# Kernel optimization log

Hardware: AMD Instinct MI355X
Metric: run time of the kernel (lower is better)

The kernel has to match this reference:

```python
import jax, jax.numpy as jnp
import numpy as np

B, L, D, H = 4, 1024, 1024, 16
HD = D // H  # head_dim = 64


def setup_inputs() -> dict:
    key = jax.random.key(0)
    k1, k2, k3, k4 = jax.random.split(key, 4)
    x = jax.random.normal(k1, (B, L, D), dtype=jnp.float32)
    # causal mask: positions where mask == 0 are filled with -inf
    mask = jnp.tril(jnp.ones((L, L), dtype=bool))[None, None, :, :]  # [1,1,L,L]
    w_qkv = jax.random.normal(k2, (D, 3 * D), dtype=jnp.float32) * (D ** -0.5)
    w_out = jax.random.normal(k3, (D, D), dtype=jnp.float32) * (D ** -0.5)
    rel_pos_bias = jax.random.normal(k4, (H, L, L), dtype=jnp.float32) * 0.02
    return {"x": x, "mask": mask, "w_qkv": w_qkv, "w_out": w_out,
            "rel_pos_bias": rel_pos_bias}


def reference(x, mask, w_qkv, w_out, rel_pos_bias):
    b, l, d = x.shape
    scale = HD ** -0.5
    qkv = (x @ w_qkv).reshape(b, l, 3, H, HD)          # [B,L,3,H,hd]
    q, k, v = qkv[:, :, 0], qkv[:, :, 1], qkv[:, :, 2]  # each [B,L,H,hd]
    # scores: [B,H,Lq,Lk]
    scores = jnp.einsum('bqhd,bkhd->bhqk', q, k) * scale
    scores = scores + rel_pos_bias[None, :, :l, :l]
    scores = jnp.where(mask, scores, -jnp.inf)
    attn = jax.nn.softmax(scores, axis=-1)  # dropout is identity in eval
    out = jnp.einsum('bhqk,bkhd->bqhd', attn, v).reshape(b, l, d)
    return out @ w_out
```

## Files before the change

kernel.cpp:

```cpp
#include <hip/hip_runtime.h>
#include <hip/hip_bf16.h>
#include <math.h>

#define B_  4
#define L_  1024
#define D_  1024
#define H_  16
#define HD_ 64
#define SCALE 0.125f
#define LOG2E 1.44269504f
#define SCALE_L2E (0.125f * 1.44269504f)
#define NEG_BIG -3.0e38f

typedef __bf16 bf16x8 __attribute__((ext_vector_type(8)));
typedef float  f32x4  __attribute__((ext_vector_type(4)));

__device__ __forceinline__ float b2f(unsigned short u) {
    union { unsigned int i; float f; } x; x.i = ((unsigned)u) << 16; return x.f;
}
__device__ __forceinline__ unsigned short f2b(float f) {
    __hip_bfloat16 h = __float2bfloat16(f);
    return *reinterpret_cast<unsigned short*>(&h);
}
__device__ __forceinline__ void gl_lds16(const void* g, void* l) {
    __builtin_amdgcn_global_load_lds(
        (const __attribute__((address_space(1))) void*)g,
        (__attribute__((address_space(3))) void*)l, 16, 0, 0);
}

__global__ __launch_bounds__(256) void prep_kernel(
    const float* __restrict__ x, const float* __restrict__ w_qkv,
    const float* __restrict__ w_out, unsigned short* __restrict__ xb,
    unsigned short* __restrict__ wqkvT, unsigned short* __restrict__ woutT)
{
    const int bid = blockIdx.x;
    if (bid < 4096) {
        int i = (bid * 256 + threadIdx.x) * 4;
        float4 v = *(const float4*)&x[i];
        ushort4 o = make_ushort4(f2b(v.x), f2b(v.y), f2b(v.z), f2b(v.w));
        *(ushort4*)&xb[i] = o;
        return;
    }
    __shared__ float tile[32][33];
    const float* w; unsigned short* wt; int N, n0, k0;
    if (bid < 7168) {
        int b2 = bid - 4096;
        w = w_qkv; wt = wqkvT; N = 3072;
        n0 = (b2 % 96) * 32; k0 = (b2 / 96) * 32;
    } else {
        int b3 = bid - 7168;
        w = w_out; wt = woutT; N = 1024;
        n0 = (b3 % 32) * 32; k0 = (b3 / 32) * 32;
    }
    const int tx = threadIdx.x & 31, ty = threadIdx.x >> 5;
#pragma unroll
    for (int i = 0; i < 4; i++) {
        int kk = ty + i * 8;
        tile[kk][tx] = w[(size_t)(k0 + kk) * N + n0 + tx];
    }
    __syncthreads();
#pragma unroll
    for (int i = 0; i < 4; i++) {
        int nn = ty + i * 8;
        wt[(size_t)(n0 + nn) * 1024 + k0 + tx] = f2b(tile[tx][nn]);
    }
}

__device__ __forceinline__ void gemm_core(
    const unsigned short* __restrict__ A, const unsigned short* __restrict__ Bt,
    unsigned short* As, unsigned short* Bs,
    int m0, int n0, int wave, int lane, int wm, int wn,
    f32x4 acc[4][4])
{
    const int srow = lane >> 2, spos = lane & 3;
    const int sc   = spos ^ ((srow >> 1) & 3);
    const int mlane = lane & 15, chunk = lane >> 4;
    const int foff  = mlane * 32 + (chunk ^ ((mlane >> 1) & 3)) * 8;

    for (int k0 = 0; k0 < 1024; k0 += 32) {
#pragma unroll
        for (int t = 0; t < 2; t++) {
            int rb = wave * 32 + t * 16;
            int r  = rb + srow;
            gl_lds16(&A [(size_t)(m0 + r) * 1024 + k0 + sc * 8], &As[rb * 32]);
            gl_lds16(&Bt[(size_t)(n0 + r) * 1024 + k0 + sc * 8], &Bs[rb * 32]);
        }
        __syncthreads();
        bf16x8 af[4], bfr[4];
#pragma unroll
        for (int i = 0; i < 4; i++) {
            af[i]  = *(const bf16x8*)&As[(wm * 64 + i * 16) * 32 + foff];
            bfr[i] = *(const bf16x8*)&Bs[(wn * 64 + i * 16) * 32 + foff];
        }
#pragma unroll
        for (int i = 0; i < 4; i++)
#pragma unroll
            for (int j = 0; j < 4; j++)
                acc[i][j] = __builtin_amdgcn_mfma_f32_16x16x32_bf16(
                    bfr[i], af[j], acc[i][j], 0, 0, 0);
        __syncthreads();
    }
}

__global__ __launch_bounds__(256) void qkv_gemm_kernel(
    const unsigned short* __restrict__ A, const unsigned short* __restrict__ Bt,
    unsigned short* __restrict__ qb, unsigned short* __restrict__ kb,
    unsigned short* __restrict__ vtb)
{
    __shared__ unsigned short As[128 * 32];
    __shared__ unsigned short Bs[128 * 32];
    const int tid  = threadIdx.x;
    const int wave = tid >> 6, lane = tid & 63;
    const int quad = lane >> 4, l16 = lane & 15;
    const int wm = wave >> 1, wn = wave & 1;
    const int m0 = blockIdx.y * 128, n0 = blockIdx.x * 128;
    f32x4 acc[4][4] = {};
    gemm_core(A, Bt, As, Bs, m0, n0, wave, lane, wm, wn, acc);

    const int s = n0 >> 10;
#pragma unroll
    for (int i = 0; i < 4; i++) {
        int n_base = n0 + wn * 64 + i * 16 + quad * 4;
        int h = (n_base >> 6) & 15, hd0 = n_base & 63;
#pragma unroll
        for (int j = 0; j < 4; j++) {
            int m = m0 + wm * 64 + j * 16 + l16;
            int b = m >> 10, l = m & 1023;
            if (s == 2) {
#pragma unroll
                for (int r = 0; r < 4; r++)
                    vtb[((size_t)((b * 16 + h) * 64 + hd0 + r)) * 1024 + l] =
                        f2b(acc[i][j][r]);
            } else {
                unsigned short* dst = (s == 0) ? qb : kb;
                unsigned short tmp[4];
#pragma unroll
                for (int r = 0; r < 4; r++) tmp[r] = f2b(acc[i][j][r]);
                *(ushort4*)&dst[(((size_t)(b * 16 + h) * 1024 + l) << 6) + hd0] =
                    *(ushort4*)tmp;
            }
        }
    }
}

__global__ __launch_bounds__(256) void out_gemm_kernel(
    const unsigned short* __restrict__ A, const unsigned short* __restrict__ Bt,
    float* __restrict__ out)
{
    __shared__ unsigned short As[128 * 32];
    __shared__ unsigned short Bs[64 * 32];
    const int tid  = threadIdx.x;
    const int wave = tid >> 6, lane = tid & 63;
    const int quad = lane >> 4, l16 = lane & 15;
    const int srow = lane >> 2, spos = lane & 3;
    const int sc   = spos ^ ((srow >> 1) & 3);
    const int mlane = lane & 15, chunk = lane >> 4;
    const int foff  = mlane * 32 + (chunk ^ ((mlane >> 1) & 3)) * 8;
    const int m0 = blockIdx.y * 128, n0 = blockIdx.x * 64;
    f32x4 acc[4][2] = {};

    for (int k0 = 0; k0 < 1024; k0 += 32) {
#pragma unroll
        for (int t = 0; t < 2; t++) {
            int rb = wave * 32 + t * 16;
            gl_lds16(&A[(size_t)(m0 + rb + srow) * 1024 + k0 + sc * 8], &As[rb * 32]);
        }
        {
            int rb = wave * 16;
            gl_lds16(&Bt[(size_t)(n0 + rb + srow) * 1024 + k0 + sc * 8], &Bs[rb * 32]);
        }
        __syncthreads();
        bf16x8 af[2], bfr[4];
#pragma unroll
        for (int i = 0; i < 2; i++)
            af[i]  = *(const bf16x8*)&As[(wave * 32 + i * 16) * 32 + foff];
#pragma unroll
        for (int j = 0; j < 4; j++)
            bfr[j] = *(const bf16x8*)&Bs[(j * 16) * 32 + foff];
#pragma unroll
        for (int jn = 0; jn < 4; jn++)
#pragma unroll
            for (int im = 0; im < 2; im++)
                acc[jn][im] = __builtin_amdgcn_mfma_f32_16x16x32_bf16(
                    bfr[jn], af[im], acc[jn][im], 0, 0, 0);
        __syncthreads();
    }
#pragma unroll
    for (int jn = 0; jn < 4; jn++) {
        int n_base = n0 + jn * 16 + quad * 4;
#pragma unroll
        for (int im = 0; im < 2; im++) {
            int m = m0 + wave * 32 + im * 16 + l16;
            float4 o = make_float4(acc[jn][im][0], acc[jn][im][1],
                                   acc[jn][im][2], acc[jn][im][3]);
            *(float4*)&out[(size_t)m * 1024 + n_base] = o;
        }
    }
}

__global__ __launch_bounds__(256, 4) void attn_mfma_kernel(
    const unsigned short* __restrict__ qb, const unsigned short* __restrict__ kb,
    const unsigned short* __restrict__ vtb, const float* __restrict__ bias,
    unsigned short* __restrict__ ob)
{
    __shared__ unsigned short Ks [2 * 64 * 72];
    __shared__ unsigned short Vts[2 * 64 * 72];
    __shared__ unsigned short Ps [64 * 72];

    const int tid  = threadIdx.x;
    const int wave = tid >> 6, lane = tid & 63;
    const int quad = lane >> 4, l16 = lane & 15;
    const int bh = blockIdx.x, b = bh >> 4, h = bh & 15;
    const int qt = 15 - blockIdx.y;
    const int q0 = qt * 64;
    const int srow = tid >> 3, scol = (tid & 7) * 8;
    const size_t qkv_base = (size_t)bh * (1024 * 64);

    const int qrow  = q0 + wave * 16;
    const int qlane = qrow + l16;

    bf16x8 a0 = *(const bf16x8*)&qb[qkv_base + (size_t)(qrow + l16) * 64 + quad * 8];
    bf16x8 a1 = *(const bf16x8*)&qb[qkv_base + (size_t)(qrow + l16) * 64 + 32 + quad * 8];

    uint4 kpre0 = *(const uint4*)&kb [qkv_base + (size_t)srow * 64 + scol];
    uint4 kpre1 = *(const uint4*)&kb [qkv_base + (size_t)(srow + 32) * 64 + scol];
    uint4 vpre0 = *(const uint4*)&vtb[qkv_base + (size_t)srow * 1024 + scol];
    uint4 vpre1 = *(const uint4*)&vtb[qkv_base + (size_t)(srow + 32) * 1024 + scol];

    const float* bias_row = &bias[((size_t)h * 1024 + qlane) * 1024];

    float bA[16], bB[16];
#pragma unroll
    for (int nt = 0; nt < 4; nt++) {
        float4 b4 = *(const float4*)&bias_row[nt * 16 + quad * 4];
        bA[nt * 4 + 0] = b4.x * LOG2E; bA[nt * 4 + 1] = b4.y * LOG2E;
        bA[nt * 4 + 2] = b4.z * LOG2E; bA[nt * 4 + 3] = b4.w * LOG2E;
    }

    float lr = 0.f;
    f32x4 O[4] = {};

    *(uint4*)&Ks [srow * 72 + scol]        = kpre0;
    *(uint4*)&Ks [(srow + 32) * 72 + scol] = kpre1;
    *(uint4*)&Vts[srow * 72 + scol]        = vpre0;
    *(uint4*)&Vts[(srow + 32) * 72 + scol] = vpre1;
    __syncthreads();

    auto tile = [&](int kt, float* bc, float* bn) {
        const bool pf = (kt < qt);
        if (pf) {
            const int kn = (kt + 1) * 64;
            kpre0 = *(const uint4*)&kb [qkv_base + (size_t)(kn + srow) * 64 + scol];
            kpre1 = *(const uint4*)&kb [qkv_base + (size_t)(kn + srow + 32) * 64 + scol];
            vpre0 = *(const uint4*)&vtb[qkv_base + (size_t)srow * 1024 + kn + scol];
            vpre1 = *(const uint4*)&vtb[qkv_base + (size_t)(srow + 32) * 1024 + kn + scol];
#pragma unroll
            for (int nt = 0; nt < 4; nt++) {
                float4 b4 = *(const float4*)&bias_row[kn + nt * 16 + quad * 4];
                bn[nt * 4 + 0] = b4.x * LOG2E; bn[nt * 4 + 1] = b4.y * LOG2E;
                bn[nt * 4 + 2] = b4.z * LOG2E; bn[nt * 4 + 3] = b4.w * LOG2E;
            }
        }
        const unsigned short* Kc = &Ks [(kt & 1) * 4608];
        const unsigned short* Vc = &Vts[(kt & 1) * 4608];
        f32x4 sacc[4] = {};
        __builtin_amdgcn_s_setprio(1);
#pragma unroll
        for (int nt = 0; nt < 4; nt++) {
            bf16x8 k0 = *(const bf16x8*)&Kc[(nt * 16 + l16) * 72 + quad * 8];
            bf16x8 k1 = *(const bf16x8*)&Kc[(nt * 16 + l16) * 72 + 32 + quad * 8];
            sacc[nt] = __builtin_amdgcn_mfma_f32_16x16x32_bf16(k0, a0, sacc[nt], 0, 0, 0);
            sacc[nt] = __builtin_amdgcn_mfma_f32_16x16x32_bf16(k1, a1, sacc[nt], 0, 0, 0);
        }
        __builtin_amdgcn_s_setprio(0);
        const bool dg = (kt == qt);
        const int kb0 = kt * 64 + quad * 4;
#pragma unroll
        for (int nt = 0; nt < 4; nt++) {
            float ps[4];
#pragma unroll
            for (int r = 0; r < 4; r++) {
                float v = fmaf(sacc[nt][r], SCALE_L2E, bc[nt * 4 + r]);
                if (dg && (kb0 + nt * 16 + r) > qlane) v = NEG_BIG;
                ps[r] = exp2f(v);
            }
            lr += (ps[0] + ps[1]) + (ps[2] + ps[3]);
            ushort4 pw = make_ushort4(f2b(ps[0]), f2b(ps[1]), f2b(ps[2]), f2b(ps[3]));
            *(ushort4*)&Ps[(wave * 16 + l16) * 72 + nt * 16 + quad * 4] = pw;
        }
        bf16x8 p0 = *(const bf16x8*)&Ps[(wave * 16 + l16) * 72 + quad * 8];
        bf16x8 p1 = *(const bf16x8*)&Ps[(wave * 16 + l16) * 72 + 32 + quad * 8];
        __builtin_amdgcn_s_setprio(1);
#pragma unroll
        for (int dt = 0; dt < 4; dt++) {
            bf16x8 v0 = *(const bf16x8*)&Vc[(dt * 16 + l16) * 72 + quad * 8];
            bf16x8 v1 = *(const bf16x8*)&Vc[(dt * 16 + l16) * 72 + 32 + quad * 8];
            O[dt] = __builtin_amdgcn_mfma_f32_16x16x32_bf16(p0, v0, O[dt], 0, 0, 0);
            O[dt] = __builtin_amdgcn_mfma_f32_16x16x32_bf16(p1, v1, O[dt], 0, 0, 0);
        }
        __builtin_amdgcn_s_setprio(0);
        if (pf) {
            unsigned short* Kn = &Ks [((kt + 1) & 1) * 4608];
            unsigned short* Vn = &Vts[((kt + 1) & 1) * 4608];
            *(uint4*)&Kn[srow * 72 + scol]        = kpre0;
            *(uint4*)&Kn[(srow + 32) * 72 + scol] = kpre1;
            *(uint4*)&Vn[srow * 72 + scol]        = vpre0;
            *(uint4*)&Vn[(srow + 32) * 72 + scol] = vpre1;
        }
        __syncthreads();
    };

    for (int kt = 0; kt <= qt; kt += 2) {
        tile(kt, bA, bB);
        if (kt + 1 <= qt) tile(kt + 1, bB, bA);
    }

    lr += __shfl_xor(lr, 16);
    lr += __shfl_xor(lr, 32);

#pragma unroll
    for (int r = 0; r < 4; r++) {
        float s = __shfl(lr, quad * 4 + r);
        float inv = 1.0f / s;
        int qgr = qrow + quad * 4 + r;
#pragma unroll
        for (int dt = 0; dt < 4; dt++)
            ob[((size_t)(b * 1024 + qgr)) * 1024 + h * 64 + dt * 16 + l16] =
                f2b(O[dt][r] * inv);
    }
}


extern "C" void kernel_launch(void* const* d_in, const int* in_sizes, int n_in,
                              void* d_out, int out_size, void* d_ws, size_t ws_size,
                              hipStream_t stream) {
    const float* x     = (const float*)d_in[0];
    const float* w_qkv = (const float*)d_in[2];
    const float* w_out = (const float*)d_in[3];
    const float* bias  = (const float*)d_in[4];
    float* out = (float*)d_out;

    char* ws = (char*)d_ws;
    unsigned short* xb     = (unsigned short*)ws;              ws += (size_t)4096 * 1024 * 2;
    unsigned short* wqkvT  = (unsigned short*)ws;              ws += (size_t)3072 * 1024 * 2;
    unsigned short* woutT  = (unsigned short*)ws;              ws += (size_t)1024 * 1024 * 2;
    unsigned short* qb     = (unsigned short*)ws;              ws += (size_t)4096 * 1024 * 2;
    unsigned short* kb     = (unsigned short*)ws;              ws += (size_t)4096 * 1024 * 2;
    unsigned short* vtb    = (unsigned short*)ws;              ws += (size_t)4096 * 1024 * 2;
    unsigned short* ab     = (unsigned short*)ws;

    prep_kernel<<<8192, 256, 0, stream>>>(x, w_qkv, w_out, xb, wqkvT, woutT);
    qkv_gemm_kernel<<<dim3(24, 32), 256, 0, stream>>>(xb, wqkvT, qb, kb, vtb);
    attn_mfma_kernel<<<dim3(64, 16), 256, 0, stream>>>(qb, kb, vtb, bias, ab);
    out_gemm_kernel<<<dim3(16, 32), 256, 0, stream>>>(ab, woutT, out);
}
```

Before: 216.5 us.

## Repack P into MFMA operand layout with lane permutes instead of LDS round-trip

```diff
diff --git a/kernel.cpp b/kernel.cpp
--- a/kernel.cpp
+++ b/kernel.cpp
@@ -205,13 +205,14 @@
 {
     __shared__ unsigned short Ks [2 * 64 * 72];
     __shared__ unsigned short Vts[2 * 64 * 72];
-    __shared__ unsigned short Ps [64 * 72];
 
     const int tid  = threadIdx.x;
     const int wave = tid >> 6, lane = tid & 63;
     const int quad = lane >> 4, l16 = lane & 15;
     const int bh = blockIdx.x, b = bh >> 4, h = bh & 15;
-    const int qt = 15 - blockIdx.y;
+    const int yk = blockIdx.y & 3, seg = blockIdx.y >> 2;
+    const int qt = (seg == 0) ? 15 - yk : (seg == 1) ? yk
+                 : (seg == 2) ? 11 - yk : yk + 4;
     const int q0 = qt * 64;
     const int srow = tid >> 3, scol = (tid & 7) * 8;
     const size_t qkv_base = (size_t)bh * (1024 * 64);
@@ -275,6 +276,7 @@
         __builtin_amdgcn_s_setprio(0);
         const bool dg = (kt == qt);
         const int kb0 = kt * 64 + quad * 4;
+        unsigned int pk[4][2];
 #pragma unroll
         for (int nt = 0; nt < 4; nt++) {
             float ps[4];
@@ -285,11 +287,27 @@
                 ps[r] = exp2f(v);
             }
             lr += (ps[0] + ps[1]) + (ps[2] + ps[3]);
-            ushort4 pw = make_ushort4(f2b(ps[0]), f2b(ps[1]), f2b(ps[2]), f2b(ps[3]));
-            *(ushort4*)&Ps[(wave * 16 + l16) * 72 + nt * 16 + quad * 4] = pw;
-        }
-        bf16x8 p0 = *(const bf16x8*)&Ps[(wave * 16 + l16) * 72 + quad * 8];
-        bf16x8 p1 = *(const bf16x8*)&Ps[(wave * 16 + l16) * 72 + 32 + quad * 8];
+            asm("v_cvt_pk_bf16_f32 %0, %1, %2"
+                : "=v"(pk[nt][0]) : "v"(ps[0]), "v"(ps[1]));
+            asm("v_cvt_pk_bf16_f32 %0, %1, %2"
+                : "=v"(pk[nt][1]) : "v"(ps[2]), "v"(ps[3]));
+        }
+        unsigned int pa[4], pb[4];
+#pragma unroll
+        for (int i = 0; i < 2; i++) {
+            unsigned int xa = pk[0][i], xb = pk[1][i];
+            asm("v_permlane32_swap_b32 %0, %1" : "+v"(xa), "+v"(xb));
+            asm("v_permlane16_swap_b32 %0, %1" : "+v"(xa), "+v"(xb));
+            pa[i] = xa; pa[2 + i] = xb;
+            unsigned int xc = pk[2][i], xd = pk[3][i];
+            asm("v_permlane32_swap_b32 %0, %1" : "+v"(xc), "+v"(xd));
+            asm("v_permlane16_swap_b32 %0, %1" : "+v"(xc), "+v"(xd));
+            pb[i] = xc; pb[2 + i] = xd;
+        }
+        union { unsigned int u[4]; bf16x8 v; } U0, U1;
+        U0.u[0] = pa[0]; U0.u[1] = pa[1]; U0.u[2] = pa[2]; U0.u[3] = pa[3];
+        U1.u[0] = pb[0]; U1.u[1] = pb[1]; U1.u[2] = pb[2]; U1.u[3] = pb[3];
+        bf16x8 p0 = U0.v, p1 = U1.v;
         __builtin_amdgcn_s_setprio(1);
 #pragma unroll
         for (int dt = 0; dt < 4; dt++) {
```

Result: no change. 216.9 us (+0.2%).
